# Performance work log

Hardware: AMD Instinct MI355X
Metric: run time of the kernel (lower is better)

Reference implementation:

```python
import jax, jax.numpy as jnp
import numpy as np

D_IN, D, K, N_CLASSES = 384, 512, 6, 2
SCALE = D ** (-0.5)

def _linear_params(key, fan_in, fan_out):
    kw, kb = jax.random.split(key)
    w = jax.random.normal(kw, (fan_in, fan_out), jnp.float32) * 0.02
    b = jax.random.normal(kb, (fan_out,), jnp.float32) * 0.01
    return w, b

def setup_inputs() -> dict:
    key = jax.random.key(0)
    ks = jax.random.split(key, 10)
    x = jax.random.normal(ks[0], (16384, D_IN), jnp.float32)
    fc1_w, fc1_b = _linear_params(ks[1], D_IN, D)
    wh_w, wh_b = _linear_params(ks[2], D, D)
    wt_w, wt_b = _linear_params(ks[3], D, D)
    lin1_w, lin1_b = _linear_params(ks[4], D, D)
    lin2_w, lin2_b = _linear_params(ks[5], D, D)
    att1_w, att1_b = _linear_params(ks[6], D, D // 2)
    att2_w, att2_b = _linear_params(ks[7], D // 2, 1)
    ln_g = jnp.ones((D,), jnp.float32)
    ln_b = jnp.zeros((D,), jnp.float32)
    fc_w, fc_b = _linear_params(ks[8], D, N_CLASSES)
    return dict(x=x, fc1_w=fc1_w, fc1_b=fc1_b, wh_w=wh_w, wh_b=wh_b,
                wt_w=wt_w, wt_b=wt_b, lin1_w=lin1_w, lin1_b=lin1_b,
                lin2_w=lin2_w, lin2_b=lin2_b, att1_w=att1_w, att1_b=att1_b,
                att2_w=att2_w, att2_b=att2_b, ln_g=ln_g, ln_b=ln_b,
                fc_w=fc_w, fc_b=fc_b)

def _forward(x, fc1_w, fc1_b, wh_w, wh_b, wt_w, wt_b, lin1_w, lin1_b,
             lin2_w, lin2_b, att1_w, att1_b, att2_w, att2_b, ln_g, ln_b,
             fc_w, fc_b):
    lrelu = jax.nn.leaky_relu  # slope 0.01, matches nn.LeakyReLU default
    h = lrelu(x @ fc1_w + fc1_b)                    # [N, D]
    h = (h + h.mean(axis=0, keepdims=True)) * 0.5
    e_h = h @ wh_w + wh_b                           # [N, D]
    e_t = h @ wt_w + wt_b                           # [N, D]
    attn_logit = (e_h * SCALE) @ e_t.T              # [N, N]
    topk_w, topk_i = jax.lax.top_k(attn_logit, K)   # [N, K]
    Nb = e_t[topk_i]                                # gather neighbors [N, K, D]
    p = jax.nn.softmax(topk_w, axis=-1)             # [N, K]
    eh_r = p[..., None] * Nb + (1.0 - p)[..., None] * e_h[:, None, :]
    gate = jnp.tanh(e_h[:, None, :] + eh_r)         # [N, K, D]
    # faithful to torch.einsum('ijkl,ijkm->ijk', Nb, gate): product of sums
    ka_w = Nb.sum(axis=-1) * gate.sum(axis=-1)      # [N, K]
    ka_p = jax.nn.softmax(ka_w, axis=-1)
    e_Nh = jnp.einsum('nk,nkd->nd', ka_p, Nb)       # [N, D]
    sum_emb = lrelu((e_h + e_Nh) @ lin1_w + lin1_b)
    bi_emb = lrelu((e_h * e_Nh) @ lin2_w + lin2_b)
    emb = sum_emb + bi_emb                          # [N, D] (dropout=eval, identity)
    # GlobalAttention readout
    a = lrelu(emb @ att1_w + att1_b) @ att2_w + att2_b  # [N, 1]
    g = jax.nn.softmax(a, axis=0)
    pooled = (g * emb).sum(axis=0, keepdims=True)   # [1, D]
    mu = pooled.mean(axis=-1, keepdims=True)
    var = pooled.var(axis=-1, keepdims=True)
    normed = (pooled - mu) * jax.lax.rsqrt(var + 1e-5) * ln_g + ln_b
    logits = normed @ fc_w + fc_b                   # [1, n_classes]
    return logits

def reference(x, fc1_w, fc1_b, wh_w, wh_b, wt_w, wt_b, lin1_w, lin1_b,
              lin2_w, lin2_b, att1_w, att1_b, att2_w, att2_b, ln_g, ln_b,
              fc_w, fc_b):
    logits = _forward(x, fc1_w, fc1_b, wh_w, wh_b, wt_w, wt_b, lin1_w, lin1_b,
                      lin2_w, lin2_b, att1_w, att1_b, att2_w, att2_b,
                      ln_g, ln_b, fc_w, fc_b)
    y_prob = jax.nn.softmax(logits, axis=-1)
    return logits, y_prob
```

## Files before the change

### kernel.cpp

```cpp
#include <hip/hip_runtime.h>
#include <math.h>

#define NROWS 16384
#define DIN   384
#define DIM   512
#define KSEL  6
#define NSPLIT 4
#define COLS_PER_SPLIT (NROWS / NSPLIT)
#define ATT_SCALE 0.044194173824159216f

typedef unsigned short u16;
typedef __attribute__((ext_vector_type(8))) short bf16x8;
typedef __attribute__((ext_vector_type(16))) float f32x16;

static __device__ __forceinline__ float lrelu_f(float v) {
  return v > 0.f ? v : 0.01f * v;
}

static __device__ __forceinline__ u16 f2bf(float f) {
  unsigned u = __float_as_uint(f);
  unsigned r = (u + 0x7FFFu + ((u >> 16) & 1u)) >> 16;
  return (u16)r;
}

static __device__ __forceinline__ void sbar() {
  asm volatile("" ::: "memory");
  __builtin_amdgcn_s_barrier();
  asm volatile("" ::: "memory");
}

__global__ __launch_bounds__(256)
void convx(const float* __restrict__ X, u16* __restrict__ Xb) {
  int i = blockIdx.x * 256 + threadIdx.x;
  const float4* p = (const float4*)X + (size_t)i * 2;
  float4 a = p[0], b = p[1];
  uint4 o;
  o.x = f2bf(a.x) | ((unsigned)f2bf(a.y) << 16);
  o.y = f2bf(a.z) | ((unsigned)f2bf(a.w) << 16);
  o.z = f2bf(b.x) | ((unsigned)f2bf(b.y) << 16);
  o.w = f2bf(b.z) | ((unsigned)f2bf(b.w) << 16);
  ((uint4*)Xb)[i] = o;
}

__global__ __launch_bounds__(256)
void wconv(const float* __restrict__ W, u16* __restrict__ Wt, int K, int N) {
  int t = blockIdx.x * 256 + threadIdx.x;
  if (t >= K * N) return;
  int k = t / N, n = t - k * N;
  Wt[(size_t)n * K + k] = f2bf(W[t]);
}

__global__ __launch_bounds__(256)
void colsum_partial(const float* __restrict__ H, float* __restrict__ part) {
  int col = blockIdx.x * 64 + (threadIdx.x & 63);
  int sub = threadIdx.x >> 6;
  int rEnd = blockIdx.y * 512 + 512;
  float s = 0.f;
  for (int r = blockIdx.y * 512 + sub; r < rEnd; r += 4)
    s += H[(size_t)r * DIM + col];
  __shared__ float sh[4][64];
  sh[sub][threadIdx.x & 63] = s;
  __syncthreads();
  if (threadIdx.x < 64) {
    float tot = sh[0][threadIdx.x] + sh[1][threadIdx.x] +
                sh[2][threadIdx.x] + sh[3][threadIdx.x];
    part[(size_t)blockIdx.y * DIM + col] = tot;
  }
}

__global__ void finalize_mean(const float* __restrict__ part,
                              float* __restrict__ mean) {
  int c = threadIdx.x;
  float s = 0.f;
  for (int j = 0; j < 32; j++) s += part[j * DIM + c];
  mean[c] = s * (1.0f / NROWS);
}

__global__ __launch_bounds__(256)
void h_fix_bf(const float* __restrict__ H0, const float* __restrict__ mean,
              u16* __restrict__ Hb) {
  int idx = blockIdx.x * 256 + threadIdx.x;
  int c = (idx * 8) & (DIM - 1);
  const float4* p = (const float4*)H0 + (size_t)idx * 2;
  float4 a = p[0], b = p[1];
  float4 m0 = *(const float4*)(mean + c);
  float4 m1 = *(const float4*)(mean + c + 4);
  a.x = (a.x + m0.x) * 0.5f; a.y = (a.y + m0.y) * 0.5f;
  a.z = (a.z + m0.z) * 0.5f; a.w = (a.w + m0.w) * 0.5f;
  b.x = (b.x + m1.x) * 0.5f; b.y = (b.y + m1.y) * 0.5f;
  b.z = (b.z + m1.z) * 0.5f; b.w = (b.w + m1.w) * 0.5f;
  uint4 o;
  o.x = f2bf(a.x) | ((unsigned)f2bf(a.y) << 16);
  o.y = f2bf(a.z) | ((unsigned)f2bf(a.w) << 16);
  o.z = f2bf(b.x) | ((unsigned)f2bf(b.y) << 16);
  o.w = f2bf(b.z) | ((unsigned)f2bf(b.w) << 16);
  ((uint4*)Hb)[idx] = o;
}

template<int ACT, int ACCUM, int STOREBF>
__global__ __launch_bounds__(256, 2)
void gemm_bf16(const u16* __restrict__ A, const u16* __restrict__ Wt,
               const float* __restrict__ bias, float* __restrict__ C,
               u16* __restrict__ Cb, float bscale, int K, int N) {
  __shared__ char lds[65536];
  const int tid = threadIdx.x;
  const int w = tid >> 6, l = tid & 63;
  const int l31 = l & 31, lh = l >> 5, lh16 = lh << 4;
  const int qg = w & 1, ng = w >> 1;
  const int swz = (l31 & 7) << 4;
  const int rowBase = blockIdx.y * 128;
  const int colBase = blockIdx.x * 128;
  const int nsteps = K >> 6;

  f32x16 z;
  #pragma unroll
  for (int i = 0; i < 16; i++) z[i] = 0.f;
  f32x16 acc00 = z, acc01 = z, acc10 = z, acc11 = z;

#define GSTAGE(buf_, kc_) do { \
    const int r_ = tid >> 3, j_ = tid & 7; \
    const int js_ = ((j_ ^ (r_ & 7)) << 3); \
    const u16* as_ = A + (size_t)rowBase * K + (kc_); \
    const u16* ws_ = Wt + (size_t)colBase * K + (kc_); \
    char* ab_ = lds + (buf_) * 16384; \
    char* wb_ = lds + 32768 + (buf_) * 16384; \
    _Pragma("unroll") \
    for (int p_ = 0; p_ < 4; ++p_) { \
      __builtin_amdgcn_global_load_lds( \
        (const __attribute__((address_space(1))) void*)(as_ + (size_t)(r_ + 32 * p_) * K + js_), \
        (__attribute__((address_space(3))) void*)(ab_ + w * 1024 + p_ * 4096), 16, 0, 0); \
      __builtin_amdgcn_global_load_lds( \
        (const __attribute__((address_space(1))) void*)(ws_ + (size_t)(r_ + 32 * p_) * K + js_), \
        (__attribute__((address_space(3))) void*)(wb_ + w * 1024 + p_ * 4096), 16, 0, 0); \
    } \
  } while (0)

  GSTAGE(0, 0);
  asm volatile("s_waitcnt vmcnt(0)" ::: "memory");
  sbar();
  #pragma unroll 1
  for (int s = 0; s < nsteps; ++s) {
    const int cur = s & 1;
    if (s + 1 < nsteps) GSTAGE(cur ^ 1, (s + 1) * 64);
    __builtin_amdgcn_sched_barrier(0);
    const char* ab = lds + cur * 16384;
    const char* wb = lds + 32768 + cur * 16384;
    __builtin_amdgcn_s_setprio(1);
    #pragma unroll
    for (int s4 = 0; s4 < 4; ++s4) {
      const int off = (s4 * 32 + lh16) ^ swz;
      bf16x8 am0 = *(const bf16x8*)(ab + (qg * 64 + l31) * 128 + off);
      bf16x8 am1 = *(const bf16x8*)(ab + (qg * 64 + 32 + l31) * 128 + off);
      bf16x8 wn0 = *(const bf16x8*)(wb + (ng * 64 + l31) * 128 + off);
      bf16x8 wn1 = *(const bf16x8*)(wb + (ng * 64 + 32 + l31) * 128 + off);
      acc00 = __builtin_amdgcn_mfma_f32_32x32x16_bf16(wn0, am0, acc00, 0, 0, 0);
      acc01 = __builtin_amdgcn_mfma_f32_32x32x16_bf16(wn1, am0, acc01, 0, 0, 0);
      acc10 = __builtin_amdgcn_mfma_f32_32x32x16_bf16(wn0, am1, acc10, 0, 0, 0);
      acc11 = __builtin_amdgcn_mfma_f32_32x32x16_bf16(wn1, am1, acc11, 0, 0, 0);
    }
    __builtin_amdgcn_s_setprio(0);
    asm volatile("s_waitcnt vmcnt(0)" ::: "memory");
    sbar();
  }
#undef GSTAGE

  float* Ls = (float*)lds;
  {
    const int m0 = qg * 64 + l31;
    const int k0 = (m0 & 7) << 2;
    #pragma unroll
    for (int r = 0; r < 16; ++r) {
      const int nd = ng * 64 + (r & 3) + 8 * (r >> 2) + 4 * lh;
      Ls[m0 * 128 + (nd ^ k0)] = acc00[r];
      Ls[m0 * 128 + ((nd + 32) ^ k0)] = acc01[r];
      Ls[(m0 + 32) * 128 + (nd ^ k0)] = acc10[r];
      Ls[(m0 + 32) * 128 + ((nd + 32) ^ k0)] = acc11[r];
    }
  }
  sbar();
  #pragma unroll
  for (int p = 0; p < 16; ++p) {
    int idx = tid + 256 * p;
    int m = idx >> 5, c4 = (idx & 31) << 2;
    float4 v = *(const float4*)&Ls[m * 128 + (c4 ^ ((m & 7) << 2))];
    int col = colBase + c4;
    float4 bv = *(const float4*)&bias[col];
    v.x += bv.x; v.y += bv.y; v.z += bv.z; v.w += bv.w;
    if (ACT) {
      v.x = lrelu_f(v.x); v.y = lrelu_f(v.y);
      v.z = lrelu_f(v.z); v.w = lrelu_f(v.w);
    }
    size_t o = (size_t)(rowBase + m) * N + col;
    if (ACCUM) {
      float4 c0 = *(const float4*)&C[o];
      v.x += c0.x; v.y += c0.y; v.z += c0.z; v.w += c0.w;
    }
    *(float4*)&C[o] = v;
    if (STOREBF) {
      ushort4 q;
      q.x = f2bf(v.x * bscale); q.y = f2bf(v.y * bscale);
      q.z = f2bf(v.z * bscale); q.w = f2bf(v.w * bscale);
      *(ushort4*)&Cb[o] = q;
    }
  }
}

#define T6(tv, tix, vv, cc) do { float v_ = (vv); \
  if (v_ > tv[5]) { tv[5] = v_; tix[5] = (cc); \
    if (tv[5] > tv[4]) { float t=tv[4];tv[4]=tv[5];tv[5]=t; int q=tix[4];tix[4]=tix[5];tix[5]=q; } \
    if (tv[4] > tv[3]) { float t=tv[3];tv[3]=tv[4];tv[4]=t; int q=tix[3];tix[3]=tix[4];tix[4]=q; } \
    if (tv[3] > tv[2]) { float t=tv[2];tv[2]=tv[3];tv[3]=t; int q=tix[2];tix[2]=tix[3];tix[3]=q; } \
    if (tv[2] > tv[1]) { float t=tv[1];tv[1]=tv[2];tv[2]=t; int q=tix[1];tix[1]=tix[2];tix[2]=q; } \
    if (tv[1] > tv[0]) { float t=tv[0];tv[0]=tv[1];tv[1]=t; int q=tix[0];tix[0]=tix[1];tix[1]=q; } \
  } } while (0)

__global__ __launch_bounds__(256, 2)
void attn_topk_mfma(const u16* __restrict__ EHb, const u16* __restrict__ ETb,
                    float* __restrict__ TWp, int* __restrict__ TIp) {
  __shared__ char lds[24576];
  const int tid = threadIdx.x;
  const int w = tid >> 6, l = tid & 63;
  const int l31 = l & 31, lh = l >> 5;

  const int bid = blockIdx.x;
  const int xcd = bid & 7;
  const int split = xcd & 3;
  const int rowBase = ((xcd >> 2) * 64 + (bid >> 3)) * 128;
  const int qrow = rowBase + w * 32 + l31;

  bf16x8 areg[32];
  {
    const u16* ap = EHb + (size_t)qrow * DIM + lh * 8;
    #pragma unroll
    for (int ks = 0; ks < 32; ++ks)
      areg[ks] = *(const bf16x8*)(ap + ks * 16);
  }

  f32x16 z;
  #pragma unroll
  for (int i = 0; i < 16; i++) z[i] = 0.f;
  f32x16 acc0 = z, acc1 = z;

  float tv[KSEL]; int tix[KSEL];
  #pragma unroll
  for (int k = 0; k < KSEL; k++) { tv[k] = -INFINITY; tix[k] = 0x7fffffff; }

#define STAGE(bufi_, ph_) do { \
    const int ct_ = (ph_) >> 3, kc_ = (ph_) & 7; \
    char* db_ = lds + (bufi_) * 8192; \
    const u16* bs_ = ETb + (size_t)(split * COLS_PER_SPLIT + ct_ * 64) * DIM + kc_ * 64; \
    _Pragma("unroll") \
    for (int p_ = 0; p_ < 2; ++p_) { \
      const int c_ = tid + 256 * p_; \
      const int rn_ = c_ >> 3; \
      const int js_ = (((c_ & 7) ^ (rn_ & 7)) << 3); \
      __builtin_amdgcn_global_load_lds( \
        (const __attribute__((address_space(1))) void*)(bs_ + (size_t)rn_ * DIM + js_), \
        (__attribute__((address_space(3))) void*)(db_ + w * 1024 + p_ * 4096), 16, 0, 0); \
    } \
  } while (0)

  int bufr = 0;
  STAGE(0, 0);
  STAGE(1, 1);
  asm volatile("s_waitcnt vmcnt(2)" ::: "memory");

  #pragma unroll 1
  for (int ct = 0; ct < 64; ++ct) {
    #pragma unroll
    for (int kc = 0; kc < 8; ++kc) {
      sbar();
      const char* db = lds + bufr * 8192;
      __builtin_amdgcn_s_setprio(1);
      #pragma unroll
      for (int s4 = 0; s4 < 4; ++s4) {
        const int c0 = ((s4 * 2 + lh) ^ (l31 & 7)) * 16;
        bf16x8 bn0 = *(const bf16x8*)(db + l31 * 128 + c0);
        const int r1 = 32 + l31;
        const int c1 = ((s4 * 2 + lh) ^ (r1 & 7)) * 16;
        bf16x8 bn1 = *(const bf16x8*)(db + r1 * 128 + c1);
        acc0 = __builtin_amdgcn_mfma_f32_32x32x16_bf16(bn0, areg[kc * 4 + s4], acc0, 0, 0, 0);
        acc1 = __builtin_amdgcn_mfma_f32_32x32x16_bf16(bn1, areg[kc * 4 + s4], acc1, 0, 0, 0);
      }
      __builtin_amdgcn_s_setprio(0);
      if (kc == 7) {
        const int cb = split * COLS_PER_SPLIT + ct * 64 + 4 * lh;
        #pragma unroll
        for (int r = 0; r < 16; ++r) {
          const int nd = cb + (r & 3) + 8 * (r >> 2);
          T6(tv, tix, acc0[r], nd);
          T6(tv, tix, acc1[r], nd + 32);
        }
        acc0 = z; acc1 = z;
      }
      __builtin_amdgcn_sched_barrier(0);
      {
        const int p = ct * 8 + kc;
        if (p + 2 < 512) {
          const int bs = (bufr >= 1) ? bufr - 1 : bufr + 2;
          STAGE(bs, p + 2);
        }
        if (p < 510) { asm volatile("s_waitcnt vmcnt(2)" ::: "memory"); }
        else         { asm volatile("s_waitcnt vmcnt(0)" ::: "memory"); }
      }
      bufr = (bufr == 2) ? 0 : bufr + 1;
    }
  }
#undef STAGE

  {
    float pv[KSEL]; int pi[KSEL];
    #pragma unroll
    for (int k = 0; k < KSEL; k++) {
      pv[k] = __shfl_xor(tv[k], 32);
      pi[k] = __shfl_xor(tix[k], 32);
    }
    #pragma unroll
    for (int k = 0; k < KSEL; k++) {
      float cv = pv[k]; int ci = pi[k];
      if ((cv > tv[5]) || (cv == tv[5] && ci < tix[5])) {
        tv[5] = cv; tix[5] = ci;
        if ((tv[5] > tv[4]) || (tv[5] == tv[4] && tix[5] < tix[4])) {
          float t = tv[4]; tv[4] = tv[5]; tv[5] = t;
          int q = tix[4]; tix[4] = tix[5]; tix[5] = q; }
        if ((tv[4] > tv[3]) || (tv[4] == tv[3] && tix[4] < tix[3])) {
          float t = tv[3]; tv[3] = tv[4]; tv[4] = t;
          int q = tix[3]; tix[3] = tix[4]; tix[4] = q; }
        if ((tv[3] > tv[2]) || (tv[3] == tv[2] && tix[3] < tix[2])) {
          float t = tv[2]; tv[2] = tv[3]; tv[3] = t;
          int q = tix[2]; tix[2] = tix[3]; tix[3] = q; }
        if ((tv[2] > tv[1]) || (tv[2] == tv[1] && tix[2] < tix[1])) {
          float t = tv[1]; tv[1] = tv[2]; tv[2] = t;
          int q = tix[1]; tix[1] = tix[2]; tix[2] = q; }
        if ((tv[1] > tv[0]) || (tv[1] == tv[0] && tix[1] < tix[0])) {
          float t = tv[0]; tv[0] = tv[1]; tv[1] = t;
          int q = tix[0]; tix[0] = tix[1]; tix[1] = q; }
      }
    }
  }
  if (lh == 0) {
    size_t o = ((size_t)split * NROWS + qrow) * KSEL;
    #pragma unroll
    for (int k = 0; k < KSEL; k++) { TWp[o + k] = tv[k]; TIp[o + k] = tix[k]; }
  }
}

__global__ __launch_bounds__(256)
void topk_merge(const float* __restrict__ TWp, const int* __restrict__ TIp,
                float* __restrict__ TW, int* __restrict__ TI) {
  int row = blockIdx.x * 256 + threadIdx.x;
  float tv[KSEL]; int tix[KSEL];
  #pragma unroll
  for (int k = 0; k < KSEL; k++) { tv[k] = -INFINITY; tix[k] = 0x7fffffff; }
  #pragma unroll
  for (int s = 0; s < NSPLIT; s++) {
    size_t o = ((size_t)s * NROWS + row) * KSEL;
    #pragma unroll
    for (int k = 0; k < KSEL; k++) {
      float cv = TWp[o + k]; int ci = TIp[o + k];
      bool better5 = (cv > tv[5]) || (cv == tv[5] && ci < tix[5]);
      if (better5) {
        tv[5] = cv; tix[5] = ci;
        if ((tv[5] > tv[4]) || (tv[5] == tv[4] && tix[5] < tix[4])) {
          float t = tv[4]; tv[4] = tv[5]; tv[5] = t;
          int ti = tix[4]; tix[4] = tix[5]; tix[5] = ti; }
        if ((tv[4] > tv[3]) || (tv[4] == tv[3] && tix[4] < tix[3])) {
          float t = tv[3]; tv[3] = tv[4]; tv[4] = t;
          int ti = tix[3]; tix[3] = tix[4]; tix[4] = ti; }
        if ((tv[3] > tv[2]) || (tv[3] == tv[2] && tix[3] < tix[2])) {
          float t = tv[2]; tv[2] = tv[3]; tv[3] = t;
          int ti = tix[2]; tix[2] = tix[3]; tix[3] = ti; }
        if ((tv[2] > tv[1]) || (tv[2] == tv[1] && tix[2] < tix[1])) {
          float t = tv[1]; tv[1] = tv[2]; tv[2] = t;
          int ti = tix[1]; tix[1] = tix[2]; tix[2] = ti; }
        if ((tv[1] > tv[0]) || (tv[1] == tv[0] && tix[1] < tix[0])) {
          float t = tv[0]; tv[0] = tv[1]; tv[1] = t;
          int ti = tix[0]; tix[0] = tix[1]; tix[1] = ti; }
      }
    }
  }
  size_t o = (size_t)row * KSEL;
  #pragma unroll
  for (int k = 0; k < KSEL; k++) { TW[o + k] = tv[k]; TI[o + k] = tix[k]; }
}

__global__ __launch_bounds__(256)
void neighbor_kernel(const float* __restrict__ EH, const float* __restrict__ ET,
                     const float* __restrict__ TW, const int* __restrict__ TI,
                     u16* __restrict__ SINb, u16* __restrict__ BINb) {
  const int lane = threadIdx.x & 63;
  const int row = blockIdx.x * 4 + (threadIdx.x >> 6);
  const float* eh = EH + (size_t)row * DIM;
  float ehv[8];
  #pragma unroll
  for (int u = 0; u < 8; u++) ehv[u] = eh[u * 64 + lane];
  float tw[KSEL]; int ti[KSEL];
  #pragma unroll
  for (int k = 0; k < KSEL; k++) {
    tw[k] = TW[(size_t)row * KSEL + k];
    ti[k] = TI[(size_t)row * KSEL + k];
  }
  float m = tw[0];
  #pragma unroll
  for (int k = 1; k < KSEL; k++) m = fmaxf(m, tw[k]);
  float p[KSEL], ps = 0.f;
  #pragma unroll
  for (int k = 0; k < KSEL; k++) { p[k] = expf(tw[k] - m); ps += p[k]; }
  float inv = 1.f / ps;
  #pragma unroll
  for (int k = 0; k < KSEL; k++) p[k] *= inv;

  float nb[KSEL][8];
  float kaw[KSEL];
  #pragma unroll
  for (int k = 0; k < KSEL; k++) {
    const float* et = ET + (size_t)ti[k] * DIM;
    float snb = 0.f, sg = 0.f;
    #pragma unroll
    for (int u = 0; u < 8; u++) {
      float nbv = et[u * 64 + lane];
      nb[k][u] = nbv;
      float ehr = p[k] * nbv + (1.f - p[k]) * ehv[u];
      float g = tanhf(ehv[u] + ehr);
      snb += nbv; sg += g;
    }
    #pragma unroll
    for (int off = 32; off > 0; off >>= 1) {
      snb += __shfl_xor(snb, off);
      sg  += __shfl_xor(sg, off);
    }
    kaw[k] = snb * sg;
  }
  float km = kaw[0];
  #pragma unroll
  for (int k = 1; k < KSEL; k++) km = fmaxf(km, kaw[k]);
  float kp[KSEL], ks = 0.f;
  #pragma unroll
  for (int k = 0; k < KSEL; k++) { kp[k] = expf(kaw[k] - km); ks += kp[k]; }
  float kinv = 1.f / ks;
  #pragma unroll
  for (int k = 0; k < KSEL; k++) kp[k] *= kinv;

  #pragma unroll
  for (int u = 0; u < 8; u++) {
    float enh = 0.f;
    #pragma unroll
    for (int k = 0; k < KSEL; k++) enh += kp[k] * nb[k][u];
    size_t o = (size_t)row * DIM + u * 64 + lane;
    SINb[o] = f2bf(ehv[u] + enh);
    BINb[o] = f2bf(ehv[u] * enh);
  }
}

__global__ __launch_bounds__(256)
void att2_kernel(const float* __restrict__ HID, const float* __restrict__ w2,
                 const float* __restrict__ b2, float* __restrict__ ASC) {
  const int lane = threadIdx.x & 63;
  const int row = blockIdx.x * 4 + (threadIdx.x >> 6);
  float4 hv = ((const float4*)(HID + (size_t)row * 256))[lane];
  float4 wv = ((const float4*)w2)[lane];
  float s = hv.x * wv.x + hv.y * wv.y + hv.z * wv.z + hv.w * wv.w;
  #pragma unroll
  for (int off = 32; off > 0; off >>= 1) s += __shfl_xor(s, off);
  if (lane == 0) ASC[row] = s + b2[0];
}

__global__ __launch_bounds__(1024)
void areduce(const float* __restrict__ ASC, float* __restrict__ stats) {
  __shared__ float sm[1024];
  int t = threadIdx.x;
  float m = -INFINITY;
  for (int i = t; i < NROWS; i += 1024) m = fmaxf(m, ASC[i]);
  sm[t] = m; __syncthreads();
  for (int s = 512; s > 0; s >>= 1) {
    if (t < s) sm[t] = fmaxf(sm[t], sm[t + s]);
    __syncthreads();
  }
  float mx = sm[0]; __syncthreads();
  float sum = 0.f;
  for (int i = t; i < NROWS; i += 1024) sum += expf(ASC[i] - mx);
  sm[t] = sum; __syncthreads();
  for (int s = 512; s > 0; s >>= 1) {
    if (t < s) sm[t] += sm[t + s];
    __syncthreads();
  }
  if (t == 0) { stats[0] = mx; stats[1] = sm[0]; }
}

__global__ __launch_bounds__(256)
void pooled_partial(const float* __restrict__ EMB, const float* __restrict__ ASC,
                    const float* __restrict__ stats, float* __restrict__ part) {
  int col = blockIdx.x * 64 + (threadIdx.x & 63);
  int sub = threadIdx.x >> 6;
  float mx = stats[0];
  int rEnd = blockIdx.y * 512 + 512;
  float s = 0.f;
  for (int r = blockIdx.y * 512 + sub; r < rEnd; r += 4)
    s += expf(ASC[r] - mx) * EMB[(size_t)r * DIM + col];
  __shared__ float sh[4][64];
  sh[sub][threadIdx.x & 63] = s;
  __syncthreads();
  if (threadIdx.x < 64) {
    float tot = sh[0][threadIdx.x] + sh[1][threadIdx.x] +
                sh[2][threadIdx.x] + sh[3][threadIdx.x];
    part[(size_t)blockIdx.y * DIM + col] = tot;
  }
}

__global__ __launch_bounds__(512)
void final_kernel(const float* __restrict__ part, const float* __restrict__ stats,
                  const float* __restrict__ ln_g, const float* __restrict__ ln_b,
                  const float* __restrict__ fc_w, const float* __restrict__ fc_b,
                  float* __restrict__ out) {
  __shared__ float sh[512];
  int t = threadIdx.x;
  float s = 0.f;
  for (int j = 0; j < 32; j++) s += part[j * DIM + t];
  float pooled = s / stats[1];
  sh[t] = pooled; __syncthreads();
  for (int off = 256; off > 0; off >>= 1) {
    if (t < off) sh[t] += sh[t + off];
    __syncthreads();
  }
  float mu = sh[0] * (1.f / DIM); __syncthreads();
  float dv = pooled - mu;
  sh[t] = dv * dv; __syncthreads();
  for (int off = 256; off > 0; off >>= 1) {
    if (t < off) sh[t] += sh[t + off];
    __syncthreads();
  }
  float var = sh[0] * (1.f / DIM); __syncthreads();
  float normed = dv * rsqrtf(var + 1e-5f) * ln_g[t] + ln_b[t];
  sh[t] = normed * fc_w[t * 2 + 0]; __syncthreads();
  for (int off = 256; off > 0; off >>= 1) {
    if (t < off) sh[t] += sh[t + off];
    __syncthreads();
  }
  float l0 = sh[0] + fc_b[0]; __syncthreads();
  sh[t] = normed * fc_w[t * 2 + 1]; __syncthreads();
  for (int off = 256; off > 0; off >>= 1) {
    if (t < off) sh[t] += sh[t + off];
    __syncthreads();
  }
  float l1 = sh[0] + fc_b[1];
  if (t == 0) {
    float mm = fmaxf(l0, l1);
    float e0 = expf(l0 - mm), e1 = expf(l1 - mm);
    float si = 1.f / (e0 + e1);
    out[0] = l0; out[1] = l1; out[2] = e0 * si; out[3] = e1 * si;
  }
}

extern "C" void kernel_launch(void* const* d_in, const int* in_sizes, int n_in,
                              void* d_out, int out_size, void* d_ws, size_t ws_size,
                              hipStream_t stream) {
  (void)in_sizes; (void)n_in; (void)out_size; (void)ws_size;
  const float* x      = (const float*)d_in[0];
  const float* fc1_w  = (const float*)d_in[1];
  const float* fc1_b  = (const float*)d_in[2];
  const float* wh_w   = (const float*)d_in[3];
  const float* wh_b   = (const float*)d_in[4];
  const float* wt_w   = (const float*)d_in[5];
  const float* wt_b   = (const float*)d_in[6];
  const float* lin1_w = (const float*)d_in[7];
  const float* lin1_b = (const float*)d_in[8];
  const float* lin2_w = (const float*)d_in[9];
  const float* lin2_b = (const float*)d_in[10];
  const float* att1_w = (const float*)d_in[11];
  const float* att1_b = (const float*)d_in[12];
  const float* att2_w = (const float*)d_in[13];
  const float* att2_b = (const float*)d_in[14];
  const float* ln_g   = (const float*)d_in[15];
  const float* ln_b   = (const float*)d_in[16];
  const float* fc_w   = (const float*)d_in[17];
  const float* fc_b   = (const float*)d_in[18];
  float* out = (float*)d_out;

  char* ws = (char*)d_ws;
  float* B0   = (float*)(ws);
  float* B1   = (float*)(ws + 33554432);
  float* B2   = (float*)(ws + 67108864);
  float* TWp  = (float*)(ws + 100663296);
  int*   TIp  = (int*)  (ws + 100663296 + 1572864);
  float* TW   = (float*)(ws + 100663296 + 3145728);
  int*   TI   = (int*)  (ws + 100663296 + 3145728 + 393216);
  float* part = (float*)(ws + 100663296 + 3145728 + 786432);
  float* mean = (float*)(ws + 100663296 + 3145728 + 786432 + 65536);
  float* ascr = (float*)(ws + 100663296 + 3145728 + 786432 + 65536 + 2048);
  float* stats= (float*)(ws + 100663296 + 3145728 + 786432 + 65536 + 2048 + 65536);
  u16*   hb   = (u16*)(ws + 104732672);
  u16*   EHb  = (u16*)(ws + 104732672 + 16777216);
  u16*   ETb  = (u16*)(ws + 104732672 + 33554432);
  u16*   WT   = (u16*)(ws + 104732672 + 50331648);
  u16* fc1t = WT;
  u16* wht  = fc1t + 196608;
  u16* wtt  = wht + 262144;
  u16* lin1t= wtt + 262144;
  u16* lin2t= lin1t + 262144;
  u16* att1t= lin2t + 262144;
  u16* xb   = (u16*)B1;
  u16* sinb = EHb;
  u16* binb = ETb;
  u16* embb = hb;

  convx<<<3072, 256, 0, stream>>>(x, xb);
  wconv<<<768, 256, 0, stream>>>(fc1_w, fc1t, 384, 512);
  wconv<<<1024, 256, 0, stream>>>(wh_w, wht, 512, 512);
  wconv<<<1024, 256, 0, stream>>>(wt_w, wtt, 512, 512);
  wconv<<<1024, 256, 0, stream>>>(lin1_w, lin1t, 512, 512);
  wconv<<<1024, 256, 0, stream>>>(lin2_w, lin2t, 512, 512);
  wconv<<<512, 256, 0, stream>>>(att1_w, att1t, 512, 256);
  gemm_bf16<1,0,0><<<dim3(4,128), 256, 0, stream>>>(xb, fc1t, fc1_b, B0, nullptr, 1.f, 384, 512);
  colsum_partial<<<dim3(8,32), 256, 0, stream>>>(B0, part);
  finalize_mean<<<1, 512, 0, stream>>>(part, mean);
  h_fix_bf<<<4096, 256, 0, stream>>>(B0, mean, hb);
  gemm_bf16<0,0,1><<<dim3(4,128), 256, 0, stream>>>(hb, wht, wh_b, B1, EHb, ATT_SCALE, 512, 512);
  gemm_bf16<0,0,1><<<dim3(4,128), 256, 0, stream>>>(hb, wtt, wt_b, B2, ETb, 1.f, 512, 512);
  attn_topk_mfma<<<512, 256, 0, stream>>>(EHb, ETb, TWp, TIp);
  topk_merge<<<64, 256, 0, stream>>>(TWp, TIp, TW, TI);
  neighbor_kernel<<<4096, 256, 0, stream>>>(B1, B2, TW, TI, sinb, binb);
  gemm_bf16<1,0,0><<<dim3(4,128), 256, 0, stream>>>(sinb, lin1t, lin1_b, B2, nullptr, 1.f, 512, 512);
  gemm_bf16<1,1,1><<<dim3(4,128), 256, 0, stream>>>(binb, lin2t, lin2_b, B2, embb, 1.f, 512, 512);
  gemm_bf16<1,0,0><<<dim3(2,128), 256, 0, stream>>>(embb, att1t, att1_b, B0, nullptr, 1.f, 512, 256);
  att2_kernel<<<4096, 256, 0, stream>>>(B0, att2_w, att2_b, ascr);
  areduce<<<1, 1024, 0, stream>>>(ascr, stats);
  pooled_partial<<<dim3(8,32), 256, 0, stream>>>(B2, ascr, stats, part);
  final_kernel<<<1, 512, 0, stream>>>(part, stats, ln_g, ln_b, fc_w, fc_b, out);
}
```

Baseline: 598.9 us.

## Double LDS stage size in attention top-k, fuse prep and topk merge kernels

The attention/top-k kernel now stages 128-wide K chunks (16 KB per buffer, three buffers at 48 KB) instead of 64-wide chunks, with a 16-way XOR swizzle. This halves the number of barriers and pipeline steps per column tile. The input and weight conversion kernels are merged into a single prep launch, and the top-k split merge is folded into the neighbor kernel, which removes two launches and one intermediate buffer. The larger LDS footprint may reduce occupancy in the dominant kernel.

```diff
diff --git a/kernel.cpp b/kernel.cpp
--- a/kernel.cpp
+++ b/kernel.cpp
@@ -29,25 +29,45 @@
   asm volatile("" ::: "memory");
 }
 
-__global__ __launch_bounds__(256)
-void convx(const float* __restrict__ X, u16* __restrict__ Xb) {
-  int i = blockIdx.x * 256 + threadIdx.x;
-  const float4* p = (const float4*)X + (size_t)i * 2;
-  float4 a = p[0], b = p[1];
-  uint4 o;
-  o.x = f2bf(a.x) | ((unsigned)f2bf(a.y) << 16);
-  o.y = f2bf(a.z) | ((unsigned)f2bf(a.w) << 16);
-  o.z = f2bf(b.x) | ((unsigned)f2bf(b.y) << 16);
-  o.w = f2bf(b.z) | ((unsigned)f2bf(b.w) << 16);
-  ((uint4*)Xb)[i] = o;
-}
-
-__global__ __launch_bounds__(256)
-void wconv(const float* __restrict__ W, u16* __restrict__ Wt, int K, int N) {
-  int t = blockIdx.x * 256 + threadIdx.x;
+static __device__ __forceinline__ void wconv_body(const float* W, u16* Wt,
+                                                  int K, int N, int t) {
   if (t >= K * N) return;
   int k = t / N, n = t - k * N;
   Wt[(size_t)n * K + k] = f2bf(W[t]);
+}
+
+__global__ __launch_bounds__(256)
+void prep(const float* __restrict__ X, u16* __restrict__ Xb,
+          const float* __restrict__ fc1_w, u16* __restrict__ fc1t,
+          const float* __restrict__ wh_w, u16* __restrict__ wht,
+          const float* __restrict__ wt_w, u16* __restrict__ wtt,
+          const float* __restrict__ lin1_w, u16* __restrict__ lin1t,
+          const float* __restrict__ lin2_w, u16* __restrict__ lin2t,
+          const float* __restrict__ att1_w, u16* __restrict__ att1t) {
+  const int b = blockIdx.x, tid = threadIdx.x;
+  if (b < 3072) {
+    int i = b * 256 + tid;
+    const float4* p = (const float4*)X + (size_t)i * 2;
+    float4 a = p[0], c = p[1];
+    uint4 o;
+    o.x = f2bf(a.x) | ((unsigned)f2bf(a.y) << 16);
+    o.y = f2bf(a.z) | ((unsigned)f2bf(a.w) << 16);
+    o.z = f2bf(c.x) | ((unsigned)f2bf(c.y) << 16);
+    o.w = f2bf(c.z) | ((unsigned)f2bf(c.w) << 16);
+    ((uint4*)Xb)[i] = o;
+  } else if (b < 3840) {
+    wconv_body(fc1_w, fc1t, 384, 512, (b - 3072) * 256 + tid);
+  } else if (b < 4864) {
+    wconv_body(wh_w, wht, 512, 512, (b - 3840) * 256 + tid);
+  } else if (b < 5888) {
+    wconv_body(wt_w, wtt, 512, 512, (b - 4864) * 256 + tid);
+  } else if (b < 6912) {
+    wconv_body(lin1_w, lin1t, 512, 512, (b - 5888) * 256 + tid);
+  } else if (b < 7936) {
+    wconv_body(lin2_w, lin2t, 512, 512, (b - 6912) * 256 + tid);
+  } else {
+    wconv_body(att1_w, att1t, 512, 256, (b - 7936) * 256 + tid);
+  }
 }
 
 __global__ __launch_bounds__(256)
@@ -217,7 +237,7 @@
 __global__ __launch_bounds__(256, 2)
 void attn_topk_mfma(const u16* __restrict__ EHb, const u16* __restrict__ ETb,
                     float* __restrict__ TWp, int* __restrict__ TIp) {
-  __shared__ char lds[24576];
+  __shared__ char lds[49152];
   const int tid = threadIdx.x;
   const int w = tid >> 6, l = tid & 63;
   const int l31 = l & 31, lh = l >> 5;
@@ -246,44 +266,44 @@
   for (int k = 0; k < KSEL; k++) { tv[k] = -INFINITY; tix[k] = 0x7fffffff; }
 
 #define STAGE(bufi_, ph_) do { \
-    const int ct_ = (ph_) >> 3, kc_ = (ph_) & 7; \
-    char* db_ = lds + (bufi_) * 8192; \
-    const u16* bs_ = ETb + (size_t)(split * COLS_PER_SPLIT + ct_ * 64) * DIM + kc_ * 64; \
+    const int ct_ = (ph_) >> 2, kc_ = (ph_) & 3; \
+    char* db_ = lds + (bufi_) * 16384; \
+    const u16* bs_ = ETb + (size_t)(split * COLS_PER_SPLIT + ct_ * 64) * DIM + kc_ * 128; \
     _Pragma("unroll") \
-    for (int p_ = 0; p_ < 2; ++p_) { \
-      const int c_ = tid + 256 * p_; \
-      const int rn_ = c_ >> 3; \
-      const int js_ = (((c_ & 7) ^ (rn_ & 7)) << 3); \
+    for (int p_ = 0; p_ < 4; ++p_) { \
+      const int c_ = (w * 4 + p_) * 64 + l; \
+      const int rn_ = c_ >> 4; \
+      const int js_ = ((c_ & 15) ^ (rn_ & 15)) << 3; \
       __builtin_amdgcn_global_load_lds( \
         (const __attribute__((address_space(1))) void*)(bs_ + (size_t)rn_ * DIM + js_), \
-        (__attribute__((address_space(3))) void*)(db_ + w * 1024 + p_ * 4096), 16, 0, 0); \
+        (__attribute__((address_space(3))) void*)(db_ + (w * 4 + p_) * 1024), 16, 0, 0); \
     } \
   } while (0)
 
   int bufr = 0;
   STAGE(0, 0);
   STAGE(1, 1);
-  asm volatile("s_waitcnt vmcnt(2)" ::: "memory");
+  asm volatile("s_waitcnt vmcnt(4)" ::: "memory");
 
   #pragma unroll 1
   for (int ct = 0; ct < 64; ++ct) {
     #pragma unroll
-    for (int kc = 0; kc < 8; ++kc) {
+    for (int kc = 0; kc < 4; ++kc) {
       sbar();
-      const char* db = lds + bufr * 8192;
+      const char* db = lds + bufr * 16384;
       __builtin_amdgcn_s_setprio(1);
       #pragma unroll
-      for (int s4 = 0; s4 < 4; ++s4) {
-        const int c0 = ((s4 * 2 + lh) ^ (l31 & 7)) * 16;
-        bf16x8 bn0 = *(const bf16x8*)(db + l31 * 128 + c0);
+      for (int s = 0; s < 8; ++s) {
+        const int j0 = ((s * 2 + lh) ^ (l31 & 15)) * 16;
+        bf16x8 bn0 = *(const bf16x8*)(db + l31 * 256 + j0);
         const int r1 = 32 + l31;
-        const int c1 = ((s4 * 2 + lh) ^ (r1 & 7)) * 16;
-        bf16x8 bn1 = *(const bf16x8*)(db + r1 * 128 + c1);
-        acc0 = __builtin_amdgcn_mfma_f32_32x32x16_bf16(bn0, areg[kc * 4 + s4], acc0, 0, 0, 0);
-        acc1 = __builtin_amdgcn_mfma_f32_32x32x16_bf16(bn1, areg[kc * 4 + s4], acc1, 0, 0, 0);
+        const int j1 = ((s * 2 + lh) ^ (r1 & 15)) * 16;
+        bf16x8 bn1 = *(const bf16x8*)(db + r1 * 256 + j1);
+        acc0 = __builtin_amdgcn_mfma_f32_32x32x16_bf16(bn0, areg[kc * 8 + s], acc0, 0, 0, 0);
+        acc1 = __builtin_amdgcn_mfma_f32_32x32x16_bf16(bn1, areg[kc * 8 + s], acc1, 0, 0, 0);
       }
       __builtin_amdgcn_s_setprio(0);
-      if (kc == 7) {
+      if (kc == 3) {
         const int cb = split * COLS_PER_SPLIT + ct * 64 + 4 * lh;
         #pragma unroll
         for (int r = 0; r < 16; ++r) {
@@ -295,12 +315,12 @@
       }
       __builtin_amdgcn_sched_barrier(0);
       {
-        const int p = ct * 8 + kc;
-        if (p + 2 < 512) {
+        const int p = ct * 4 + kc;
+        if (p + 2 < 256) {
           const int bs = (bufr >= 1) ? bufr - 1 : bufr + 2;
           STAGE(bs, p + 2);
         }
-        if (p < 510) { asm volatile("s_waitcnt vmcnt(2)" ::: "memory"); }
+        if (p < 254) { asm volatile("s_waitcnt vmcnt(4)" ::: "memory"); }
         else         { asm volatile("s_waitcnt vmcnt(0)" ::: "memory"); }
       }
       bufr = (bufr == 2) ? 0 : bufr + 1;
@@ -346,47 +366,8 @@
 }
 
 __global__ __launch_bounds__(256)
-void topk_merge(const float* __restrict__ TWp, const int* __restrict__ TIp,
-                float* __restrict__ TW, int* __restrict__ TI) {
-  int row = blockIdx.x * 256 + threadIdx.x;
-  float tv[KSEL]; int tix[KSEL];
-  #pragma unroll
-  for (int k = 0; k < KSEL; k++) { tv[k] = -INFINITY; tix[k] = 0x7fffffff; }
-  #pragma unroll
-  for (int s = 0; s < NSPLIT; s++) {
-    size_t o = ((size_t)s * NROWS + row) * KSEL;
-    #pragma unroll
-    for (int k = 0; k < KSEL; k++) {
-      float cv = TWp[o + k]; int ci = TIp[o + k];
-      bool better5 = (cv > tv[5]) || (cv == tv[5] && ci < tix[5]);
-      if (better5) {
-        tv[5] = cv; tix[5] = ci;
-        if ((tv[5] > tv[4]) || (tv[5] == tv[4] && tix[5] < tix[4])) {
-          float t = tv[4]; tv[4] = tv[5]; tv[5] = t;
-          int ti = tix[4]; tix[4] = tix[5]; tix[5] = ti; }
-        if ((tv[4] > tv[3]) || (tv[4] == tv[3] && tix[4] < tix[3])) {
-          float t = tv[3]; tv[3] = tv[4]; tv[4] = t;
-          int ti = tix[3]; tix[3] = tix[4]; tix[4] = ti; }
-        if ((tv[3] > tv[2]) || (tv[3] == tv[2] && tix[3] < tix[2])) {
-          float t = tv[2]; tv[2] = tv[3]; tv[3] = t;
-          int ti = tix[2]; tix[2] = tix[3]; tix[3] = ti; }
-        if ((tv[2] > tv[1]) || (tv[2] == tv[1] && tix[2] < tix[1])) {
-          float t = tv[1]; tv[1] = tv[2]; tv[2] = t;
-          int ti = tix[1]; tix[1] = tix[2]; tix[2] = ti; }
-        if ((tv[1] > tv[0]) || (tv[1] == tv[0] && tix[1] < tix[0])) {
-          float t = tv[0]; tv[0] = tv[1]; tv[1] = t;
-          int ti = tix[0]; tix[0] = tix[1]; tix[1] = ti; }
-      }
-    }
-  }
-  size_t o = (size_t)row * KSEL;
-  #pragma unroll
-  for (int k = 0; k < KSEL; k++) { TW[o + k] = tv[k]; TI[o + k] = tix[k]; }
-}
-
-__global__ __launch_bounds__(256)
 void neighbor_kernel(const float* __restrict__ EH, const float* __restrict__ ET,
-                     const float* __restrict__ TW, const int* __restrict__ TI,
+                     const float* __restrict__ TWp, const int* __restrict__ TIp,
                      u16* __restrict__ SINb, u16* __restrict__ BINb) {
   const int lane = threadIdx.x & 63;
   const int row = blockIdx.x * 4 + (threadIdx.x >> 6);
@@ -394,12 +375,37 @@
   float ehv[8];
   #pragma unroll
   for (int u = 0; u < 8; u++) ehv[u] = eh[u * 64 + lane];
+
   float tw[KSEL]; int ti[KSEL];
   #pragma unroll
-  for (int k = 0; k < KSEL; k++) {
-    tw[k] = TW[(size_t)row * KSEL + k];
-    ti[k] = TI[(size_t)row * KSEL + k];
-  }
+  for (int k = 0; k < KSEL; k++) { tw[k] = -INFINITY; ti[k] = 0x7fffffff; }
+  #pragma unroll
+  for (int s = 0; s < NSPLIT; s++) {
+    size_t o = ((size_t)s * NROWS + row) * KSEL;
+    #pragma unroll
+    for (int k = 0; k < KSEL; k++) {
+      float cv = TWp[o + k]; int ci = TIp[o + k];
+      if ((cv > tw[5]) || (cv == tw[5] && ci < ti[5])) {
+        tw[5] = cv; ti[5] = ci;
+        if ((tw[5] > tw[4]) || (tw[5] == tw[4] && ti[5] < ti[4])) {
+          float t = tw[4]; tw[4] = tw[5]; tw[5] = t;
+          int q = ti[4]; ti[4] = ti[5]; ti[5] = q; }
+        if ((tw[4] > tw[3]) || (tw[4] == tw[3] && ti[4] < ti[3])) {
+          float t = tw[3]; tw[3] = tw[4]; tw[4] = t;
+          int q = ti[3]; ti[3] = ti[4]; ti[4] = q; }
+        if ((tw[3] > tw[2]) || (tw[3] == tw[2] && ti[3] < ti[2])) {
+          float t = tw[2]; tw[2] = tw[3]; tw[3] = t;
+          int q = ti[2]; ti[2] = ti[3]; ti[3] = q; }
+        if ((tw[2] > tw[1]) || (tw[2] == tw[1] && ti[2] < ti[1])) {
+          float t = tw[1]; tw[1] = tw[2]; tw[2] = t;
+          int q = ti[1]; ti[1] = ti[2]; ti[2] = q; }
+        if ((tw[1] > tw[0]) || (tw[1] == tw[0] && ti[1] < ti[0])) {
+          float t = tw[0]; tw[0] = tw[1]; tw[1] = t;
+          int q = ti[0]; ti[0] = ti[1]; ti[1] = q; }
+      }
+    }
+  }
+
   float m = tw[0];
   #pragma unroll
   for (int k = 1; k < KSEL; k++) m = fmaxf(m, tw[k]);
@@ -582,8 +588,6 @@
   float* B2   = (float*)(ws + 67108864);
   float* TWp  = (float*)(ws + 100663296);
   int*   TIp  = (int*)  (ws + 100663296 + 1572864);
-  float* TW   = (float*)(ws + 100663296 + 3145728);
-  int*   TI   = (int*)  (ws + 100663296 + 3145728 + 393216);
   float* part = (float*)(ws + 100663296 + 3145728 + 786432);
   float* mean = (float*)(ws + 100663296 + 3145728 + 786432 + 65536);
   float* ascr = (float*)(ws + 100663296 + 3145728 + 786432 + 65536 + 2048);
@@ -603,13 +607,8 @@
   u16* binb = ETb;
   u16* embb = hb;
 
-  convx<<<3072, 256, 0, stream>>>(x, xb);
-  wconv<<<768, 256, 0, stream>>>(fc1_w, fc1t, 384, 512);
-  wconv<<<1024, 256, 0, stream>>>(wh_w, wht, 512, 512);
-  wconv<<<1024, 256, 0, stream>>>(wt_w, wtt, 512, 512);
-  wconv<<<1024, 256, 0, stream>>>(lin1_w, lin1t, 512, 512);
-  wconv<<<1024, 256, 0, stream>>>(lin2_w, lin2t, 512, 512);
-  wconv<<<512, 256, 0, stream>>>(att1_w, att1t, 512, 256);
+  prep<<<8448, 256, 0, stream>>>(x, xb, fc1_w, fc1t, wh_w, wht, wt_w, wtt,
+                                 lin1_w, lin1t, lin2_w, lin2t, att1_w, att1t);
   gemm_bf16<1,0,0><<<dim3(4,128), 256, 0, stream>>>(xb, fc1t, fc1_b, B0, nullptr, 1.f, 384, 512);
   colsum_partial<<<dim3(8,32), 256, 0, stream>>>(B0, part);
   finalize_mean<<<1, 512, 0, stream>>>(part, mean);
@@ -617,8 +616,7 @@
   gemm_bf16<0,0,1><<<dim3(4,128), 256, 0, stream>>>(hb, wht, wh_b, B1, EHb, ATT_SCALE, 512, 512);
   gemm_bf16<0,0,1><<<dim3(4,128), 256, 0, stream>>>(hb, wtt, wt_b, B2, ETb, 1.f, 512, 512);
   attn_topk_mfma<<<512, 256, 0, stream>>>(EHb, ETb, TWp, TIp);
-  topk_merge<<<64, 256, 0, stream>>>(TWp, TIp, TW, TI);
-  neighbor_kernel<<<4096, 256, 0, stream>>>(B1, B2, TW, TI, sinb, binb);
+  neighbor_kernel<<<4096, 256, 0, stream>>>(B1, B2, TWp, TIp, sinb, binb);
   gemm_bf16<1,0,0><<<dim3(4,128), 256, 0, stream>>>(sinb, lin1t, lin1_b, B2, nullptr, 1.f, 512, 512);
   gemm_bf16<1,1,1><<<dim3(4,128), 256, 0, stream>>>(binb, lin2t, lin2_b, B2, embb, 1.f, 512, 512);
   gemm_bf16<1,0,0><<<dim3(2,128), 256, 0, stream>>>(embb, att1t, att1_b, B0, nullptr, 1.f, 512, 256);
```

Result: no change. 602.8 us (+0.6%).
